# Optimization experiments

Measured on AMD Instinct MI355X. Metric: run time of the kernel, lower is better.

Reference implementation:

```python
import jax, jax.numpy as jnp
import numpy as np

C_IN = 64
GDIM = C_IN // 2      # 32, GHPA dim_in
CD = GDIM // 4        # 8, c_dim_in
GRID = C_IN // 2      # 32, learned param grid (x=y)
EXPR = 2
B, W, H, D = 2, 64, 64, 64


def _gelu(x):
    return jax.nn.gelu(x, approximate=False)


def _interp_last(p, out_len):
    # 1D linear interpolation along last axis, align_corners=True
    L = p.shape[-1]
    pos = jnp.linspace(0.0, L - 1.0, out_len)
    i0 = jnp.clip(jnp.floor(pos).astype(jnp.int32), 0, L - 1)
    i1 = jnp.clip(i0 + 1, 0, L - 1)
    w = (pos - i0).astype(p.dtype)
    return p[..., i0] * (1.0 - w) + p[..., i1] * w


def _interp2(p, h, w):
    # bilinear align_corners=True over last two axes (separable)
    p = _interp_last(p, w)
    p = jnp.swapaxes(_interp_last(jnp.swapaxes(p, -2, -1), h), -2, -1)
    return p


def _conv2d(x, w, b, groups=1, pad=0):
    y = jax.lax.conv_general_dilated(x, w, (1, 1), [(pad, pad), (pad, pad)],
                                     feature_group_count=groups,
                                     dimension_numbers=('NCHW', 'OIHW', 'NCHW'))
    return y + b[None, :, None, None]


def _conv1d(x, w, b, groups=1, pad=0):
    y = jax.lax.conv_general_dilated(x, w, (1,), [(pad, pad)],
                                     feature_group_count=groups,
                                     dimension_numbers=('NCH', 'OIH', 'NCH'))
    return y + b[None, :, None]


def _ln_cf(x, g, b, eps=1e-6):
    # channels_first LayerNorm over channel axis 1 of NCHW
    u = x.mean(1, keepdims=True)
    s = ((x - u) ** 2).mean(1, keepdims=True)
    xh = (x - u) / jnp.sqrt(s + eps)
    return g[None, :, None, None] * xh + b[None, :, None, None]


def _inorm3d(x, eps=1e-5):
    # InstanceNorm3d, affine=False: normalize over spatial dims per (B, C)
    u = x.mean((2, 3, 4), keepdims=True)
    v = ((x - u) ** 2).mean((2, 3, 4), keepdims=True)
    return (x - u) / jnp.sqrt(v + eps)


def setup_inputs() -> dict:
    key = jax.random.key(0)
    ks = iter(jax.random.split(key, 40))
    f = lambda shape: 0.05 * jax.random.normal(next(ks), shape, dtype=jnp.float32)
    z = lambda shape: jnp.zeros(shape, jnp.float32)
    o = lambda shape: jnp.ones(shape, jnp.float32)
    inp = {
        'x': jax.random.normal(next(ks), (B, C_IN, W, H, D), dtype=jnp.float32),
        # GHPA layer norms
        'n1_g': o((GDIM,)), 'n1_b': z((GDIM,)),
        'n2_g': o((GDIM,)), 'n2_b': z((GDIM,)),
        # learned Hadamard params (torch inits to ones)
        'p_xy': o((1, CD, GRID, GRID)),
        'p_zx': o((1, 1, CD, GRID)),
        'p_zy': o((1, 1, CD, GRID)),
        # conv_xy: depthwise 3x3 + 1x1
        'xy_dw_w': f((CD, 1, 3, 3)), 'xy_dw_b': z((CD,)),
        'xy_pw_w': f((CD, CD, 1, 1)), 'xy_pw_b': z((CD,)),
        # conv_zx / conv_zy: depthwise 1d k=3 + 1x1 1d
        'zx_dw_w': f((CD, 1, 3)), 'zx_dw_b': z((CD,)),
        'zx_pw_w': f((CD, CD, 1)), 'zx_pw_b': z((CD,)),
        'zy_dw_w': f((CD, 1, 3)), 'zy_dw_b': z((CD,)),
        'zy_pw_w': f((CD, CD, 1)), 'zy_pw_b': z((CD,)),
        # dw branch: 1x1 + depthwise 3x3
        'dw_pw_w': f((CD, CD, 1, 1)), 'dw_pw_b': z((CD,)),
        'dw_dw_w': f((CD, 1, 3, 3)), 'dw_dw_b': z((CD,)),
        # ldw: depthwise 3x3 + 1x1 on full GDIM
        'ldw_dw_w': f((GDIM, 1, 3, 3)), 'ldw_dw_b': z((GDIM,)),
        'ldw_pw_w': f((GDIM, GDIM, 1, 1)), 'ldw_pw_b': z((GDIM,)),
        # MlpChannel 1x1x1 convs as dense over channel
        'fc1_w': f((C_IN * EXPR, C_IN)), 'fc1_b': z((C_IN * EXPR,)),
        'fc2_w': f((C_IN, C_IN * EXPR)), 'fc2_b': z((C_IN,)),
    }
    return inp


def reference(x, n1_g, n1_b, n2_g, n2_b, p_xy, p_zx, p_zy,
              xy_dw_w, xy_dw_b, xy_pw_w, xy_pw_b,
              zx_dw_w, zx_dw_b, zx_pw_w, zx_pw_b,
              zy_dw_w, zy_dw_b, zy_pw_w, zy_pw_b,
              dw_pw_w, dw_pw_b, dw_dw_w, dw_dw_b,
              ldw_dw_w, ldw_dw_b, ldw_pw_w, ldw_pw_b,
              fc1_w, fc1_b, fc2_w, fc2_b):
    cd = CD

    def ghpa(z):  # z: (N, GDIM, A, Bd)
        N, C, A, Bd = z.shape
        z = _ln_cf(z, n1_g, n1_b)
        x1, x2, x3, x4 = jnp.split(z, 4, axis=1)
        # xy branch: interpolate learned 2D grid, conv, Hadamard
        k = _interp2(p_xy, A, Bd)                       # (1, cd, A, Bd)
        k = _conv2d(k, xy_dw_w, xy_dw_b, groups=cd, pad=1)
        k = _conv2d(_gelu(k), xy_pw_w, xy_pw_b)
        x1 = x1 * k
        # zx branch: permute (N,cd,A,Bd)->(N,Bd,cd,A)
        x2p = jnp.transpose(x2, (0, 3, 1, 2))
        kz = _interp2(p_zx, cd, A)[0]                   # (1, cd, A)
        kz = _conv1d(kz, zx_dw_w, zx_dw_b, groups=cd, pad=1)
        kz = _conv1d(_gelu(kz), zx_pw_w, zx_pw_b)
        x2 = jnp.transpose(x2p * kz[None], (0, 2, 3, 1))
        # zy branch: permute (N,cd,A,Bd)->(N,A,cd,Bd)
        x3p = jnp.transpose(x3, (0, 2, 1, 3))
        ky = _interp2(p_zy, cd, Bd)[0]                  # (1, cd, Bd)
        ky = _conv1d(ky, zy_dw_w, zy_dw_b, groups=cd, pad=1)
        ky = _conv1d(_gelu(ky), zy_pw_w, zy_pw_b)
        x3 = jnp.transpose(x3p * ky[None], (0, 2, 1, 3))
        # dw branch
        x4 = _conv2d(x4, dw_pw_w, dw_pw_b)
        x4 = _conv2d(_gelu(x4), dw_dw_w, dw_dw_b, groups=cd, pad=1)
        z = jnp.concatenate([x1, x2, x3, x4], axis=1)
        z = _ln_cf(z, n2_g, n2_b)
        z = _conv2d(z, ldw_dw_w, ldw_dw_b, groups=GDIM, pad=1)
        z = _conv2d(_gelu(z), ldw_pw_w, ldw_pw_b)
        return z

    xh, xres = jnp.split(x, 2, axis=1)                  # each (B, GDIM, W, H, D)
    xh = _inorm3d(xh)
    Bb, C, Ww, Hh, Dd = xh.shape
    # direction 0: 'b c w h d -> (h b) c w d'
    xr = jnp.transpose(xh, (3, 0, 1, 2, 4)).reshape(Hh * Bb, C, Ww, Dd)
    y1 = ghpa(xr).reshape(Hh, Bb, C, Ww, Dd).transpose(1, 2, 3, 0, 4)
    y2 = ghpa(xr[::-1]).reshape(Hh, Bb, C, Ww, Dd).transpose(1, 2, 3, 0, 4)[::-1]
    whd = y1 + y2
    z = jnp.concatenate([whd, xres], axis=1)            # (B, C_IN, W, H, D)
    z = _inorm3d(z)
    # MlpChannel: 1x1x1 convs = channel-wise dense
    h = jnp.einsum('bcwhd,oc->bowhd', z, fc1_w) + fc1_b[None, :, None, None, None]
    h = _gelu(h)
    out = jnp.einsum('bcwhd,oc->bowhd', h, fc2_w) + fc2_b[None, :, None, None, None]
    return out
```

## Files before the change

### kernel.cpp

```cpp
#include <hip/hip_runtime.h>
#include <hip/hip_bf16.h>

typedef __hip_bfloat16 bf16;
typedef __attribute__((ext_vector_type(8))) short short8;
typedef __attribute__((ext_vector_type(4))) float f32x4;

__device__ __forceinline__ float b2f(bf16 v){ return __bfloat162float(v); }
__device__ __forceinline__ bf16  f2b(float v){ return __float2bfloat16(v); }
__device__ __forceinline__ unsigned short f2bu(float f){
  return __builtin_bit_cast(unsigned short, __float2bfloat16(f));
}
__device__ __forceinline__ float u2f(unsigned short u){
  return __uint_as_float(((unsigned int)u) << 16);
}
__device__ __forceinline__ float geluf(float x){ return 0.5f*x*(1.0f+erff(x*0.70710678118654752440f)); }

template<bool F32> __device__ __forceinline__ float ldin(const void* p, size_t i){
  if (F32) return ((const float*)p)[i];
  return b2f(((const bf16*)p)[i]);
}
__device__ __forceinline__ float ldf(const void* p, size_t i, bool f32){
  return f32 ? ((const float*)p)[i] : b2f(((const bf16*)p)[i]);
}

#define SS    4096
#define SSS   262144

__global__ void k_probe(const unsigned short* __restrict__ xr, int* __restrict__ flag){
  float m = 0.f;
  for (int i = threadIdx.x; i < 512; i += 64){
    unsigned int u = ((unsigned int)xr[i]) << 16;
    float v = fabsf(__uint_as_float(u));
    if (!(v < 3.0e38f)) v = 3.0e38f;
    m = fmaxf(m, v);
  }
  #pragma unroll
  for (int off = 32; off > 0; off >>= 1) m = fmaxf(m, __shfl_down(m, off));
  if (threadIdx.x == 0) flag[0] = (m > 1000.0f) ? 1 : 0;
}

__device__ __forceinline__ void blk_reduce2(float& s, float& s2){
  __shared__ float sa[4], sb[4];
  #pragma unroll
  for (int off = 32; off > 0; off >>= 1){ s += __shfl_down(s, off); s2 += __shfl_down(s2, off); }
  int wid = threadIdx.x >> 6;
  if ((threadIdx.x & 63) == 0){ sa[wid] = s; sb[wid] = s2; }
  __syncthreads();
  if (threadIdx.x == 0){ s = sa[0]+sa[1]+sa[2]+sa[3]; s2 = sb[0]+sb[1]+sb[2]+sb[3]; }
}

__global__ __launch_bounds__(256) void k_cstats(const int* __restrict__ flag,
    const void* __restrict__ x, float* __restrict__ part){
  const bool f32 = (flag[0] != 0);
  int bc = blockIdx.x >> 3, sp = blockIdx.x & 7;
  size_t base = (size_t)bc*SSS + (size_t)sp*32768;
  float s = 0.f, s2 = 0.f;
  if (f32){
    const float4* p = (const float4*)((const float*)x + base);
    for (int i = threadIdx.x; i < 8192; i += 256){
      float4 v = p[i];
      s += v.x+v.y+v.z+v.w; s2 += v.x*v.x+v.y*v.y+v.z*v.z+v.w*v.w;
    }
  } else {
    const ushort4* p = (const ushort4*)((const unsigned short*)x + base);
    for (int i = threadIdx.x; i < 8192; i += 256){
      ushort4 v = p[i];
      float a=u2f(v.x),b_=u2f(v.y),c=u2f(v.z),d=u2f(v.w);
      s += a+b_+c+d; s2 += a*a+b_*b_+c*c+d*d;
    }
  }
  blk_reduce2(s, s2);
  if (threadIdx.x == 0){ part[blockIdx.x*2] = s; part[blockIdx.x*2+1] = s2; }
}

__global__ void k_sfinal(const float* __restrict__ part,
    float* __restrict__ meanH, float* __restrict__ rstdH,
    float* __restrict__ mean2, float* __restrict__ rstd2){
  int t = threadIdx.x; if (t >= 128) return;
  float s = 0.f, s2 = 0.f;
  #pragma unroll
  for (int i = 0; i < 8; i++){ s += part[(t*8+i)*2]; s2 += part[(t*8+i)*2+1]; }
  float m = s * (1.f/262144.f);
  float var = s2 * (1.f/262144.f) - m*m;
  int b = t >> 6, c = t & 63;
  if (c < 32){ meanH[b*32+c] = m; rstdH[b*32+c] = rsqrtf(var + 1e-5f); }
  else       { mean2[t] = m;      rstd2[t] = rsqrtf(var + 1e-5f); }
}

__global__ __launch_bounds__(256) void k_mult1(const int* __restrict__ flag,
    const void* __restrict__ p_xy, const void* __restrict__ p_zx, const void* __restrict__ p_zy,
    const void* __restrict__ xy_dw_w, const void* __restrict__ xy_dw_b,
    const void* __restrict__ zx_dw_w, const void* __restrict__ zx_dw_b,
    const void* __restrict__ zy_dw_w, const void* __restrict__ zy_dw_b,
    float* __restrict__ t_xy, float* __restrict__ t_zx, float* __restrict__ t_zy){
  const bool f32 = (flag[0] != 0);
  const float SC = 31.f/63.f;
  int id = blockIdx.x*256 + threadIdx.x;
  if (id < 32768){
    int c = id >> 12, rem = id & 4095, uu = rem >> 6, vv = rem & 63;
    float acc = ldf(xy_dw_b, c, f32);
    for (int du = 0; du < 3; du++){
      int ui = uu + du - 1; if (ui < 0 || ui >= 64) continue;
      float pu = ui*SC; int i0 = (int)pu; float wu = pu - (float)i0; int i1 = min(i0+1, 31);
      for (int dv = 0; dv < 3; dv++){
        int vi = vv + dv - 1; if (vi < 0 || vi >= 64) continue;
        float pv = vi*SC; int j0 = (int)pv; float wv = pv - (float)j0; int j1 = min(j0+1, 31);
        float s = ldf(p_xy, c*1024+i0*32+j0, f32)*(1.f-wu)*(1.f-wv) + ldf(p_xy, c*1024+i0*32+j1, f32)*(1.f-wu)*wv
                + ldf(p_xy, c*1024+i1*32+j0, f32)*wu*(1.f-wv)       + ldf(p_xy, c*1024+i1*32+j1, f32)*wu*wv;
        acc += ldf(xy_dw_w, c*9 + du*3 + dv, f32) * s;
      }
    }
    t_xy[id] = geluf(acc);
  } else if (id < 33280){
    int k = id - 32768; int c = k >> 6, a = k & 63;
    float acc = ldf(zx_dw_b, c, f32);
    for (int da = 0; da < 3; da++){
      int ai = a + da - 1; if (ai < 0 || ai >= 64) continue;
      float pa = ai*SC; int i0 = (int)pa; float wa = pa - (float)i0; int i1 = min(i0+1, 31);
      float s = ldf(p_zx, c*32+i0, f32)*(1.f-wa) + ldf(p_zx, c*32+i1, f32)*wa;
      acc += ldf(zx_dw_w, c*3+da, f32) * s;
    }
    t_zx[k] = geluf(acc);
  } else if (id < 33792){
    int k = id - 33280; int c = k >> 6, a = k & 63;
    float acc = ldf(zy_dw_b, c, f32);
    for (int da = 0; da < 3; da++){
      int ai = a + da - 1; if (ai < 0 || ai >= 64) continue;
      float pa = ai*SC; int i0 = (int)pa; float wa = pa - (float)i0; int i1 = min(i0+1, 31);
      float s = ldf(p_zy, c*32+i0, f32)*(1.f-wa) + ldf(p_zy, c*32+i1, f32)*wa;
      acc += ldf(zy_dw_w, c*3+da, f32) * s;
    }
    t_zy[k] = geluf(acc);
  }
}

__global__ __launch_bounds__(256) void k_mult2(const int* __restrict__ flag,
    const float* __restrict__ t_xy, const float* __restrict__ t_zx, const float* __restrict__ t_zy,
    const void* __restrict__ xy_pw_w, const void* __restrict__ xy_pw_b,
    const void* __restrict__ zx_pw_w, const void* __restrict__ zx_pw_b,
    const void* __restrict__ zy_pw_w, const void* __restrict__ zy_pw_b,
    float* __restrict__ kxy, float* __restrict__ kz, float* __restrict__ ky){
  const bool f32 = (flag[0] != 0);
  int id = blockIdx.x*256 + threadIdx.x;
  if (id < 32768){
    int oc = id >> 12, pix = id & 4095;
    float acc = ldf(xy_pw_b, oc, f32);
    #pragma unroll
    for (int ic = 0; ic < 8; ic++) acc += ldf(xy_pw_w, oc*8+ic, f32) * t_xy[ic*4096 + pix];
    kxy[id] = acc;
  } else if (id < 33280){
    int k = id - 32768; int oc = k >> 6, a = k & 63;
    float acc = ldf(zx_pw_b, oc, f32);
    #pragma unroll
    for (int ic = 0; ic < 8; ic++) acc += ldf(zx_pw_w, oc*8+ic, f32) * t_zx[ic*64 + a];
    kz[k] = acc;
  } else if (id < 33792){
    int k = id - 33280; int oc = k >> 6, a = k & 63;
    float acc = ldf(zy_pw_b, oc, f32);
    #pragma unroll
    for (int ic = 0; ic < 8; ic++) acc += ldf(zy_pw_w, oc*8+ic, f32) * t_zy[ic*64 + a];
    ky[k] = acc;
  }
}

#define TB 4
#define W_M    0
#define W_R    32
#define W_G1   64
#define W_B1   96
#define W_G2   128
#define W_B2   160
#define W_LDWB 192
#define W_LPWB 224
#define W_PW   256
#define W_PWB  320
#define W_DW   328
#define W_DWB  400
#define W_LDW  408
#define W_LPW  696
#define W_TOT  1720

template<bool F32>
__global__ __launch_bounds__(256) void k_g(const int* __restrict__ flag,
    const void* __restrict__ x,
    const void* n1g_, const void* n1b_, const void* n2g_, const void* n2b_,
    const void* dwpw_w, const void* dwpw_b, const void* dwdw_w, const void* dwdw_b,
    const void* ldw_dw_w, const void* ldw_dw_b, const void* ldw_pw_w, const void* ldw_pw_b,
    const float* __restrict__ meanH, const float* __restrict__ rstdH,
    const float* __restrict__ kxy, const float* __restrict__ kz, const float* __restrict__ ky,
    bf16* __restrict__ g){
  if (flag[0] != (F32 ? 1 : 0)) return;
  __shared__ unsigned short xs[32*8*64];
  __shared__ unsigned short t4g[8*8*64];
  __shared__ float sw[W_TOT];
  int n  = blockIdx.x >> 4;
  int a0 = (blockIdx.x & 15) * TB;
  int b = n & 1, h = n >> 1;
  int t = threadIdx.x;
  if (t < 32){
    sw[W_M+t]=meanH[b*32+t]; sw[W_R+t]=rstdH[b*32+t];
    sw[W_G1+t]=ldin<F32>(n1g_, t); sw[W_B1+t]=ldin<F32>(n1b_, t);
    sw[W_G2+t]=ldin<F32>(n2g_, t); sw[W_B2+t]=ldin<F32>(n2b_, t);
    sw[W_LDWB+t]=ldin<F32>(ldw_dw_b, t); sw[W_LPWB+t]=ldin<F32>(ldw_pw_b, t);
  }
  if (t >= 64 && t < 128) sw[W_PW+t-64]=ldin<F32>(dwpw_w, t-64);
  if (t >= 128 && t < 200) sw[W_DW+t-128]=ldin<F32>(dwdw_w, t-128);
  if (t >= 200 && t < 208) sw[W_PWB+t-200]=ldin<F32>(dwpw_b, t-200);
  if (t >= 208 && t < 216) sw[W_DWB+t-208]=ldin<F32>(dwdw_b, t-208);
  for (int i = t; i < 288; i += 256)  sw[W_LDW+i] = ldin<F32>(ldw_dw_w, i);
  for (int i = t; i < 1024; i += 256) sw[W_LPW+i] = ldin<F32>(ldw_pw_w, i);
  __syncthreads();
  const float* s_g1 = sw+W_G1; const float* s_b1 = sw+W_B1;
  const float* s_g2 = sw+W_G2; const float* s_b2 = sw+W_B2;
  const int arow0 = a0 - 2;
  const size_t xbase = (size_t)b*64*SSS + (size_t)h*64;

  for (int i = t; i < 4096; i += 256){
    int c = i >> 7, row = (i >> 4) & 7, q = i & 15;
    int a = arow0 + row;
    unsigned short o0=0,o1=0,o2=0,o3=0;
    if (a >= 0 && a < 64){
      float m = sw[W_M+c], r = sw[W_R+c];
      size_t base = xbase + (size_t)c*SSS + (size_t)a*SS + q*4;
      if (F32){
        float4 v = *(const float4*)((const float*)x + base);
        o0=f2bu((v.x-m)*r); o1=f2bu((v.y-m)*r); o2=f2bu((v.z-m)*r); o3=f2bu((v.w-m)*r);
      } else {
        ushort4 v = *(const ushort4*)((const unsigned short*)x + base);
        o0=f2bu((u2f(v.x)-m)*r); o1=f2bu((u2f(v.y)-m)*r); o2=f2bu((u2f(v.z)-m)*r); o3=f2bu((u2f(v.w)-m)*r);
      }
    }
    ushort4 o4; o4.x=o0; o4.y=o1; o4.z=o2; o4.w=o3;
    *(ushort4*)&xs[(c*8+row)*64 + q*4] = o4;
  }
  __syncthreads();

  for (int p = t; p < 8*64; p += 256){
    int row = p >> 6, d = p & 63;
    int a = arow0 + row;
    if (a < 0 || a >= 64){
      #pragma unroll
      for (int ic = 0; ic < 8; ic++) t4g[(ic*8+row)*64+d] = 0;
      continue;
    }
    float sum = 0.f, sq = 0.f;
    #pragma unroll
    for (int c = 0; c < 32; c++){
      float v = u2f(xs[(c*8+row)*64+d]); sum += v; sq += v*v;
    }
    float mu = sum * (1.f/32.f);
    float inv = rsqrtf(sq*(1.f/32.f) - mu*mu + 1e-6f);
    float zl[8];
    #pragma unroll
    for (int j = 0; j < 8; j++){
      float v = u2f(xs[((24+j)*8+row)*64+d]);
      zl[j] = (v-mu)*inv*s_g1[24+j] + s_b1[24+j];
    }
    #pragma unroll
    for (int ic = 0; ic < 8; ic++){
      float acc = sw[W_PWB+ic];
      #pragma unroll
      for (int j = 0; j < 8; j++) acc += sw[W_PW+ic*8+j]*zl[j];
      t4g[(ic*8+row)*64+d] = f2bu(geluf(acc));
    }
  }
  __syncthreads();

  for (int p = t; p < 6*64; p += 256){
    int r2 = p >> 6, d = p & 63;
    int a = a0 - 1 + r2;
    if (a < 0 || a >= 64) continue;
    int row = r2 + 1;
    float sum = 0.f, sq = 0.f;
    #pragma unroll
    for (int c = 0; c < 32; c++){
      float v = u2f(xs[(c*8+row)*64+d]); sum += v; sq += v*v;
    }
    float mu = sum * (1.f/32.f);
    float inv = rsqrtf(sq*(1.f/32.f) - mu*mu + 1e-6f);
    float s2 = 0.f, q2 = 0.f;
    #pragma unroll
    for (int c = 0; c < 8; c++){
      int idx = (c*8+row)*64+d;
      float u = ((u2f(xs[idx])-mu)*inv*s_g1[c] + s_b1[c]) * kxy[(c*64 + a)*64 + d];
      xs[idx] = f2bu(u); s2 += u; q2 += u*u;
    }
    #pragma unroll
    for (int c = 8; c < 16; c++){
      int idx = (c*8+row)*64+d;
      float u = ((u2f(xs[idx])-mu)*inv*s_g1[c] + s_b1[c]) * kz[(c-8)*64 + a];
      xs[idx] = f2bu(u); s2 += u; q2 += u*u;
    }
    #pragma unroll
    for (int c = 16; c < 24; c++){
      int idx = (c*8+row)*64+d;
      float u = ((u2f(xs[idx])-mu)*inv*s_g1[c] + s_b1[c]) * ky[(c-16)*64 + d];
      xs[idx] = f2bu(u); s2 += u; q2 += u*u;
    }
    #pragma unroll
    for (int oc = 0; oc < 8; oc++){
      float acc = sw[W_DWB+oc];
      #pragma unroll
      for (int du = 0; du < 3; du++){
        #pragma unroll
        for (int dv = 0; dv < 3; dv++){
          int v2 = d + dv - 1;
          if (v2 >= 0 && v2 < 64) acc += sw[W_DW+oc*9+du*3+dv]*u2f(t4g[(oc*8+r2+du)*64+v2]);
        }
      }
      xs[((24+oc)*8+row)*64+d] = f2bu(acc); s2 += acc; q2 += acc*acc;
    }
    float mu2 = s2 * (1.f/32.f);
    float inv2 = rsqrtf(q2*(1.f/32.f) - mu2*mu2 + 1e-6f);
    #pragma unroll
    for (int c = 0; c < 32; c++){
      int idx = (c*8+row)*64+d;
      float uu = u2f(xs[idx]);
      xs[idx] = f2bu((uu-mu2)*inv2*s_g2[c] + s_b2[c]);
    }
  }
  __syncthreads();

  {
    int r = t >> 6, d = t & 63;
    int a = a0 + r;
    float gd[32];
    #pragma unroll
    for (int oc = 0; oc < 32; oc++){
      float acc = sw[W_LDWB+oc];
      #pragma unroll
      for (int du = 0; du < 3; du++){
        #pragma unroll
        for (int dv = 0; dv < 3; dv++){
          int v2 = d + dv - 1;
          if (v2 >= 0 && v2 < 64) acc += sw[W_LDW+oc*9+du*3+dv]*u2f(xs[(oc*8+r+1+du)*64+v2]);
        }
      }
      gd[oc] = geluf(acc);
    }
    bf16* gp = g + (size_t)n*131072 + (size_t)a*64 + d;
    #pragma unroll
    for (int o = 0; o < 32; o++){
      float acc = sw[W_LPWB+o];
      #pragma unroll
      for (int ic = 0; ic < 32; ic++) acc += sw[W_LPW+o*32+ic]*gd[ic];
      gp[(size_t)o*4096] = f2b(acc);
    }
  }
}

__global__ __launch_bounds__(256) void k_gstats(const bf16* __restrict__ g,
                                                float* __restrict__ partg){
  int pair = blockIdx.x >> 3, sp = blockIdx.x & 7;
  int b = pair >> 5, c = pair & 31;
  float s = 0.f, s2 = 0.f;
  for (int i = threadIdx.x; i < 32768; i += 256){
    int ii = sp*32768 + i;
    int d = ii & 63, w = (ii >> 6) & 63, h = ii >> 12;
    int n1 = h*2 + b, n2 = (63-h)*2 + b;
    float v = b2f(g[((size_t)n1*32 + c)*4096 + w*64 + d]) + b2f(g[((size_t)n2*32 + c)*4096 + w*64 + d]);
    s += v; s2 += v*v;
  }
  blk_reduce2(s, s2);
  if (threadIdx.x == 0){ partg[blockIdx.x*2] = s; partg[blockIdx.x*2+1] = s2; }
}

__global__ void k_gfinal(const float* __restrict__ partg,
                         float* __restrict__ mean2, float* __restrict__ rstd2){
  int t = threadIdx.x; if (t >= 64) return;
  float s = 0.f, s2 = 0.f;
  #pragma unroll
  for (int i = 0; i < 8; i++){ s += partg[(t*8+i)*2]; s2 += partg[(t*8+i)*2+1]; }
  float m = s * (1.f/262144.f);
  float var = s2 * (1.f/262144.f) - m*m;
  int b = t >> 5, c = t & 31;
  mean2[b*64+c] = m; rstd2[b*64+c] = rsqrtf(var + 1e-5f);
}

__global__ __launch_bounds__(256) void k_mlp(const int* __restrict__ flag,
    const void* __restrict__ x, const bf16* __restrict__ g,
    const float* __restrict__ mean2, const float* __restrict__ rstd2,
    const void* __restrict__ fc1w, const void* __restrict__ fc1b,
    const void* __restrict__ fc2w, const void* __restrict__ fc2b,
    void* __restrict__ out){
  const bool f32 = (flag[0] != 0);
  __shared__ unsigned short zs[128*72];
  __shared__ unsigned short w1s[128*72];
  __shared__ unsigned short w2s[64*136];
  __shared__ unsigned short hb[4*16*136];
  __shared__ float b1s[128], b2s[64];
  int blk = blockIdx.x;
  int b = blk >> 11, w = (blk >> 5) & 63, hblk = blk & 31;
  int h0 = hblk*2;
  int t = threadIdx.x;
  const float* m2 = mean2 + b*64;
  const float* r2 = rstd2 + b*64;

  if (f32){
    const float* W1 = (const float*)fc1w;
    const float* W2 = (const float*)fc2w;
    for (int i = t; i < 8192; i += 256){ int j = i >> 6, c = i & 63; w1s[j*72+c] = f2bu(W1[i] * r2[c]); }
    for (int i = t; i < 8192; i += 256){ int o = i >> 7, j = i & 127; w2s[o*136+j] = f2bu(W2[i]); }
    if (t < 128){
      float s = 0.f;
      for (int c = 0; c < 64; c++) s += W1[t*64+c] * m2[c] * r2[c];
      b1s[t] = ((const float*)fc1b)[t] - s;
    }
    if (t < 64) b2s[t] = ((const float*)fc2b)[t];
  } else {
    const bf16* W1 = (const bf16*)fc1w;
    const bf16* W2 = (const bf16*)fc2w;
    for (int i = t; i < 8192; i += 256){ int j = i >> 6, c = i & 63; w1s[j*72+c] = f2bu(b2f(W1[i]) * r2[c]); }
    for (int i = t; i < 8192; i += 256){ int o = i >> 7, j = i & 127; w2s[o*136+j] = f2bu(b2f(W2[i])); }
    if (t < 128){
      float s = 0.f;
      for (int c = 0; c < 64; c++) s += b2f(W1[t*64+c]) * m2[c] * r2[c];
      b1s[t] = b2f(((const bf16*)fc1b)[t]) - s;
    }
    if (t < 64) b2s[t] = b2f(((const bf16*)fc2b)[t]);
  }

  {
    int px = t & 127, half = t >> 7;
    int hh = px >> 6, d = px & 63;
    int h = h0 + hh;
    unsigned short tmp[32];
    if (half == 0){
      int n1 = h*2 + b, n2 = (63-h)*2 + b;
      const bf16* g1 = g + ((size_t)n1*32)*4096 + w*64 + d;
      const bf16* g2 = g + ((size_t)n2*32)*4096 + w*64 + d;
      #pragma unroll
      for (int c = 0; c < 32; c++) tmp[c] = f2bu(b2f(g1[(size_t)c*4096]) + b2f(g2[(size_t)c*4096]));
    } else {
      size_t xi = ((size_t)(b*64+32))*SSS + (size_t)w*4096 + (size_t)h*64 + d;
      if (f32){
        const float* xp = (const float*)x;
        #pragma unroll
        for (int c = 0; c < 32; c++) tmp[c] = f2bu(xp[xi + (size_t)c*SSS]);
      } else {
        const unsigned short* xp = (const unsigned short*)x;
        #pragma unroll
        for (int c = 0; c < 32; c++) tmp[c] = xp[xi + (size_t)c*SSS];
      }
    }
    short8* dst = (short8*)&zs[px*72 + half*32];
    #pragma unroll
    for (int q = 0; q < 4; q++) dst[q] = *(short8*)&tmp[q*8];
  }
  __syncthreads();

  int wv = t >> 6, l = t & 63;
  int lr = l & 15, lg = l >> 4;
  unsigned short* hbw = &hb[wv*16*136];
  #pragma unroll
  for (int mi = 0; mi < 2; mi++){
    int px0 = wv*32 + mi*16;
    short8 a0 = *(const short8*)&zs[(px0+lr)*72 + lg*8];
    short8 a1 = *(const short8*)&zs[(px0+lr)*72 + 32 + lg*8];
    f32x4 acc[8];
    #pragma unroll
    for (int jt = 0; jt < 8; jt++){
      short8 b0 = *(const short8*)&w1s[(jt*16+lr)*72 + lg*8];
      short8 b1 = *(const short8*)&w1s[(jt*16+lr)*72 + 32 + lg*8];
      f32x4 c4 = {0.f,0.f,0.f,0.f};
      c4 = __builtin_amdgcn_mfma_f32_16x16x32_bf16(a0, b0, c4, 0, 0, 0);
      c4 = __builtin_amdgcn_mfma_f32_16x16x32_bf16(a1, b1, c4, 0, 0, 0);
      acc[jt] = c4;
    }
    #pragma unroll
    for (int jt = 0; jt < 8; jt++){
      float bj = b1s[jt*16+lr];
      #pragma unroll
      for (int r = 0; r < 4; r++){
        hbw[(lg*4+r)*136 + jt*16 + lr] = f2bu(geluf(acc[jt][r] + bj));
      }
    }
    short8 ha[4];
    #pragma unroll
    for (int m = 0; m < 4; m++) ha[m] = *(const short8*)&hbw[lr*136 + m*32 + lg*8];
    #pragma unroll
    for (int ot = 0; ot < 4; ot++){
      f32x4 c4 = {0.f,0.f,0.f,0.f};
      #pragma unroll
      for (int m = 0; m < 4; m++){
        short8 bb = *(const short8*)&w2s[(ot*16+lr)*136 + m*32 + lg*8];
        c4 = __builtin_amdgcn_mfma_f32_16x16x32_bf16(ha[m], bb, c4, 0, 0, 0);
      }
      int oc = ot*16 + lr;
      float bo = b2s[oc];
      if (f32){
        float* op = (float*)out;
        #pragma unroll
        for (int r = 0; r < 4; r++){
          int px = px0 + lg*4 + r;
          size_t oi = ((size_t)(b*64+oc))*SSS + (size_t)w*4096 + (size_t)(h0 + (px>>6))*64 + (px&63);
          op[oi] = c4[r] + bo;
        }
      } else {
        bf16* op = (bf16*)out;
        #pragma unroll
        for (int r = 0; r < 4; r++){
          int px = px0 + lg*4 + r;
          size_t oi = ((size_t)(b*64+oc))*SSS + (size_t)w*4096 + (size_t)(h0 + (px>>6))*64 + (px&63);
          op[oi] = f2b(c4[r] + bo);
        }
      }
    }
  }
}

extern "C" void kernel_launch(void* const* d_in, const int* in_sizes, int n_in,
                              void* d_out, int out_size, void* d_ws, size_t ws_size,
                              hipStream_t stream) {
  const void* X      = d_in[0];
  const void* n1g    = d_in[1];
  const void* n1b    = d_in[2];
  const void* n2g    = d_in[3];
  const void* n2b    = d_in[4];
  const void* p_xy   = d_in[5];
  const void* p_zx   = d_in[6];
  const void* p_zy   = d_in[7];
  const void* xy_dw_w= d_in[8];
  const void* xy_dw_b= d_in[9];
  const void* xy_pw_w= d_in[10];
  const void* xy_pw_b= d_in[11];
  const void* zx_dw_w= d_in[12];
  const void* zx_dw_b= d_in[13];
  const void* zx_pw_w= d_in[14];
  const void* zx_pw_b= d_in[15];
  const void* zy_dw_w= d_in[16];
  const void* zy_dw_b= d_in[17];
  const void* zy_pw_w= d_in[18];
  const void* zy_pw_b= d_in[19];
  const void* dw_pw_w= d_in[20];
  const void* dw_pw_b= d_in[21];
  const void* dw_dw_w= d_in[22];
  const void* dw_dw_b= d_in[23];
  const void* ldw_dw_w=d_in[24];
  const void* ldw_dw_b=d_in[25];
  const void* ldw_pw_w=d_in[26];
  const void* ldw_pw_b=d_in[27];
  const void* fc1w   = d_in[28];
  const void* fc1b   = d_in[29];
  const void* fc2w   = d_in[30];
  const void* fc2b   = d_in[31];

  int*  flag = (int*)d_ws;
  bf16* g    = (bf16*)((char*)d_ws + 16);
  float* fb  = (float*)((char*)d_ws + 16 + (size_t)16777216*2);
  float* meanH = fb;
  float* rstdH = fb + 64;
  float* t_xy  = fb + 128;
  float* t_zx  = fb + 32896;
  float* t_zy  = fb + 33408;
  float* kxy   = fb + 33920;
  float* kz    = fb + 66688;
  float* ky    = fb + 67200;
  float* mean2 = fb + 67712;
  float* rstd2 = fb + 67840;
  float* part  = fb + 67968;
  float* partg = fb + 70016;

  k_probe<<<1, 64, 0, stream>>>((const unsigned short*)X, flag);
  k_cstats<<<1024, 256, 0, stream>>>(flag, X, part);
  k_sfinal<<<1, 128, 0, stream>>>(part, meanH, rstdH, mean2, rstd2);
  k_mult1<<<132, 256, 0, stream>>>(flag, p_xy, p_zx, p_zy, xy_dw_w, xy_dw_b,
                                   zx_dw_w, zx_dw_b, zy_dw_w, zy_dw_b, t_xy, t_zx, t_zy);
  k_mult2<<<132, 256, 0, stream>>>(flag, t_xy, t_zx, t_zy, xy_pw_w, xy_pw_b,
                                   zx_pw_w, zx_pw_b, zy_pw_w, zy_pw_b, kxy, kz, ky);
  k_g<false><<<128*(64/TB), 256, 0, stream>>>(flag, X, n1g, n1b, n2g, n2b,
                                       dw_pw_w, dw_pw_b, dw_dw_w, dw_dw_b,
                                       ldw_dw_w, ldw_dw_b, ldw_pw_w, ldw_pw_b,
                                       meanH, rstdH, kxy, kz, ky, g);
  k_g<true ><<<128*(64/TB), 256, 0, stream>>>(flag, X, n1g, n1b, n2g, n2b,
                                       dw_pw_w, dw_pw_b, dw_dw_w, dw_dw_b,
                                       ldw_dw_w, ldw_dw_b, ldw_pw_w, ldw_pw_b,
                                       meanH, rstdH, kxy, kz, ky, g);
  k_gstats<<<512, 256, 0, stream>>>(g, partg);
  k_gfinal<<<1, 64, 0, stream>>>(partg, mean2, rstd2);
  k_mlp<<<4096, 256, 0, stream>>>(flag, X, g, mean2, rstd2, fc1w, fc1b, fc2w, fc2b, d_out);
}
```

Baseline: 392.7 us.

## Use MFMA for final pointwise conv and shrink LDS halo in k_g

The final 32x32 pointwise conv in k_g moves from per-thread scalar FMAs to bf16 MFMA 16x16x32, with activations and weights staged in padded LDS buffers. The xs tile is cut from 8 to 6 rows. The two outer halo rows needed only by the dw branch are now read directly from global memory. The first-stage LayerNorm mean and rstd are cached in LDS so the second stage does not recompute them. This lowers LDS footprint and ALU work, at the cost of extra syncs, bf16 rounding of the GELU outputs before the matmul, and scattered 2-byte global stores.

```diff
diff --git a/kernel.cpp b/kernel.cpp
--- a/kernel.cpp
+++ b/kernel.cpp
@@ -177,8 +177,7 @@
 #define W_DW   328
 #define W_DWB  400
 #define W_LDW  408
-#define W_LPW  696
-#define W_TOT  1720
+#define W_TOT  696
 
 template<bool F32>
 __global__ __launch_bounds__(256) void k_g(const int* __restrict__ flag,
@@ -190,8 +189,9 @@
     const float* __restrict__ kxy, const float* __restrict__ kz, const float* __restrict__ ky,
     bf16* __restrict__ g){
   if (flag[0] != (F32 ? 1 : 0)) return;
-  __shared__ unsigned short xs[32*8*64];
+  __shared__ unsigned short xs[32*6*64];
   __shared__ unsigned short t4g[8*8*64];
+  __shared__ float muinv[2*6*64];
   __shared__ float sw[W_TOT];
   int n  = blockIdx.x >> 4;
   int a0 = (blockIdx.x & 15) * TB;
@@ -208,16 +208,15 @@
   if (t >= 200 && t < 208) sw[W_PWB+t-200]=ldin<F32>(dwpw_b, t-200);
   if (t >= 208 && t < 216) sw[W_DWB+t-208]=ldin<F32>(dwdw_b, t-208);
   for (int i = t; i < 288; i += 256)  sw[W_LDW+i] = ldin<F32>(ldw_dw_w, i);
-  for (int i = t; i < 1024; i += 256) sw[W_LPW+i] = ldin<F32>(ldw_pw_w, i);
   __syncthreads();
   const float* s_g1 = sw+W_G1; const float* s_b1 = sw+W_B1;
   const float* s_g2 = sw+W_G2; const float* s_b2 = sw+W_B2;
   const int arow0 = a0 - 2;
   const size_t xbase = (size_t)b*64*SSS + (size_t)h*64;
 
-  for (int i = t; i < 4096; i += 256){
-    int c = i >> 7, row = (i >> 4) & 7, q = i & 15;
-    int a = arow0 + row;
+  for (int i = t; i < 3072; i += 256){
+    int c = i / 96, rem = i - c*96, row = rem >> 4, q = rem & 15;
+    int a = a0 - 1 + row;
     unsigned short o0=0,o1=0,o2=0,o3=0;
     if (a >= 0 && a < 64){
       float m = sw[W_M+c], r = sw[W_R+c];
@@ -231,7 +230,7 @@
       }
     }
     ushort4 o4; o4.x=o0; o4.y=o1; o4.z=o2; o4.w=o3;
-    *(ushort4*)&xs[(c*8+row)*64 + q*4] = o4;
+    *(ushort4*)&xs[(c*6+row)*64 + q*4] = o4;
   }
   __syncthreads();
 
@@ -243,19 +242,31 @@
       for (int ic = 0; ic < 8; ic++) t4g[(ic*8+row)*64+d] = 0;
       continue;
     }
-    float sum = 0.f, sq = 0.f;
-    #pragma unroll
-    for (int c = 0; c < 32; c++){
-      float v = u2f(xs[(c*8+row)*64+d]); sum += v; sq += v*v;
+    float sum = 0.f, sq = 0.f; float z24[8];
+    if (row >= 1 && row <= 6){
+      int r6 = row - 1;
+      #pragma unroll
+      for (int c = 0; c < 32; c++){
+        float v = u2f(xs[(c*6+r6)*64+d]); sum += v; sq += v*v;
+        if (c >= 24) z24[c-24] = v;
+      }
+    } else {
+      size_t xi = xbase + (size_t)a*SS + d;
+      #pragma unroll
+      for (int c = 0; c < 32; c++){
+        float v = (ldin<F32>(x, xi + (size_t)c*SSS) - sw[W_M+c]) * sw[W_R+c];
+        sum += v; sq += v*v;
+        if (c >= 24) z24[c-24] = v;
+      }
     }
     float mu = sum * (1.f/32.f);
     float inv = rsqrtf(sq*(1.f/32.f) - mu*mu + 1e-6f);
+    if (row >= 1 && row <= 6){
+      muinv[(row-1)*64+d] = mu; muinv[384 + (row-1)*64+d] = inv;
+    }
     float zl[8];
     #pragma unroll
-    for (int j = 0; j < 8; j++){
-      float v = u2f(xs[((24+j)*8+row)*64+d]);
-      zl[j] = (v-mu)*inv*s_g1[24+j] + s_b1[24+j];
-    }
+    for (int j = 0; j < 8; j++) zl[j] = (z24[j]-mu)*inv*s_g1[24+j] + s_b1[24+j];
     #pragma unroll
     for (int ic = 0; ic < 8; ic++){
       float acc = sw[W_PWB+ic];
@@ -270,30 +281,23 @@
     int r2 = p >> 6, d = p & 63;
     int a = a0 - 1 + r2;
     if (a < 0 || a >= 64) continue;
-    int row = r2 + 1;
-    float sum = 0.f, sq = 0.f;
-    #pragma unroll
-    for (int c = 0; c < 32; c++){
-      float v = u2f(xs[(c*8+row)*64+d]); sum += v; sq += v*v;
-    }
-    float mu = sum * (1.f/32.f);
-    float inv = rsqrtf(sq*(1.f/32.f) - mu*mu + 1e-6f);
+    float mu = muinv[r2*64+d], inv = muinv[384 + r2*64+d];
     float s2 = 0.f, q2 = 0.f;
     #pragma unroll
     for (int c = 0; c < 8; c++){
-      int idx = (c*8+row)*64+d;
+      int idx = (c*6+r2)*64+d;
       float u = ((u2f(xs[idx])-mu)*inv*s_g1[c] + s_b1[c]) * kxy[(c*64 + a)*64 + d];
       xs[idx] = f2bu(u); s2 += u; q2 += u*u;
     }
     #pragma unroll
     for (int c = 8; c < 16; c++){
-      int idx = (c*8+row)*64+d;
+      int idx = (c*6+r2)*64+d;
       float u = ((u2f(xs[idx])-mu)*inv*s_g1[c] + s_b1[c]) * kz[(c-8)*64 + a];
       xs[idx] = f2bu(u); s2 += u; q2 += u*u;
     }
     #pragma unroll
     for (int c = 16; c < 24; c++){
-      int idx = (c*8+row)*64+d;
+      int idx = (c*6+r2)*64+d;
       float u = ((u2f(xs[idx])-mu)*inv*s_g1[c] + s_b1[c]) * ky[(c-16)*64 + d];
       xs[idx] = f2bu(u); s2 += u; q2 += u*u;
     }
@@ -308,23 +312,28 @@
           if (v2 >= 0 && v2 < 64) acc += sw[W_DW+oc*9+du*3+dv]*u2f(t4g[(oc*8+r2+du)*64+v2]);
         }
       }
-      xs[((24+oc)*8+row)*64+d] = f2bu(acc); s2 += acc; q2 += acc*acc;
+      xs[((24+oc)*6+r2)*64+d] = f2bu(acc); s2 += acc; q2 += acc*acc;
     }
     float mu2 = s2 * (1.f/32.f);
     float inv2 = rsqrtf(q2*(1.f/32.f) - mu2*mu2 + 1e-6f);
     #pragma unroll
     for (int c = 0; c < 32; c++){
-      int idx = (c*8+row)*64+d;
+      int idx = (c*6+r2)*64+d;
       float uu = u2f(xs[idx]);
       xs[idx] = f2bu((uu-mu2)*inv2*s_g2[c] + s_b2[c]);
     }
   }
   __syncthreads();
 
+  unsigned short* lpwB = t4g;
+  unsigned short* gdXS = xs;
+  for (int i = t; i < 1024; i += 256){
+    int o = i >> 5, ic = i & 31;
+    lpwB[o*40 + ic] = f2bu(ldin<F32>(ldw_pw_w, o*32+ic));
+  }
+  float gd[32];
   {
     int r = t >> 6, d = t & 63;
-    int a = a0 + r;
-    float gd[32];
     #pragma unroll
     for (int oc = 0; oc < 32; oc++){
       float acc = sw[W_LDWB+oc];
@@ -333,18 +342,44 @@
         #pragma unroll
         for (int dv = 0; dv < 3; dv++){
           int v2 = d + dv - 1;
-          if (v2 >= 0 && v2 < 64) acc += sw[W_LDW+oc*9+du*3+dv]*u2f(xs[(oc*8+r+1+du)*64+v2]);
+          if (v2 >= 0 && v2 < 64) acc += sw[W_LDW+oc*9+du*3+dv]*u2f(xs[(oc*6+r+du)*64+v2]);
         }
       }
       gd[oc] = geluf(acc);
     }
-    bf16* gp = g + (size_t)n*131072 + (size_t)a*64 + d;
-    #pragma unroll
-    for (int o = 0; o < 32; o++){
-      float acc = sw[W_LPWB+o];
-      #pragma unroll
-      for (int ic = 0; ic < 32; ic++) acc += sw[W_LPW+o*32+ic]*gd[ic];
-      gp[(size_t)o*4096] = f2b(acc);
+  }
+  __syncthreads();
+
+  #pragma unroll
+  for (int q = 0; q < 4; q++){
+    unsigned short tmp8[8];
+    #pragma unroll
+    for (int j = 0; j < 8; j++) tmp8[j] = f2bu(gd[q*8+j]);
+    *(short8*)&gdXS[t*40 + q*8] = *(const short8*)tmp8;
+  }
+  __syncthreads();
+
+  {
+    int wv = t >> 6, l = t & 63;
+    int lr = l & 15, lg = l >> 4;
+    #pragma unroll
+    for (int mi = 0; mi < 4; mi++){
+      int px0 = wv*64 + mi*16;
+      short8 af = *(const short8*)&gdXS[(px0+lr)*40 + lg*8];
+      #pragma unroll
+      for (int ot = 0; ot < 2; ot++){
+        short8 bf = *(const short8*)&lpwB[(ot*16+lr)*40 + lg*8];
+        f32x4 c4 = {0.f,0.f,0.f,0.f};
+        c4 = __builtin_amdgcn_mfma_f32_16x16x32_bf16(af, bf, c4, 0, 0, 0);
+        int oc = ot*16 + lr;
+        float bo = sw[W_LPWB+oc];
+        #pragma unroll
+        for (int r4 = 0; r4 < 4; r4++){
+          int px = px0 + lg*4 + r4;
+          int aa = a0 + (px >> 6), dd = px & 63;
+          g[(size_t)n*131072 + (size_t)oc*4096 + aa*64 + dd] = f2b(c4[r4] + bo);
+        }
+      }
     }
   }
 }
```

Measured after the change: 376.6 us. 4.1% less time.
